# Kernel tuning notes

Hardware: AMD Instinct MI355X
Metric: run time of the kernel (lower is better)

The kernel has to match this reference:

```python
import jax, jax.numpy as jnp
import numpy as np

N_QUBITS = 8
N_LAYERS = 4
DIM = 2 ** N_QUBITS  # 256 state-vector

# PauliZ sign table: signs[i, idx] = +1 if bit of wire i in basis index idx is 0 else -1.
# Wire 0 is the most-significant axis (state axes ordered wire0..wire{n-1}).
_idx = np.arange(DIM)
SIGNS = np.stack([1.0 - 2.0 * ((_idx >> (N_QUBITS - 1 - i)) & 1) for i in range(N_QUBITS)]).astype(np.float32)  # [n, 256]


def _rx_mat(theta):
    c = jnp.cos(0.5 * theta).astype(jnp.complex64)
    s = (-1j * jnp.sin(0.5 * theta)).astype(jnp.complex64)
    return jnp.stack([jnp.stack([c, s]), jnp.stack([s, c])])  # [2,2]


def _rz_diag(theta):
    return jnp.stack([jnp.exp(-0.5j * theta), jnp.exp(0.5j * theta)]).astype(jnp.complex64)  # [2]


def _apply_1q(state, U, w):
    # state: (2,)*n complex64; apply 2x2 U on wire w
    st = jnp.moveaxis(state, w, 0).reshape(2, -1)
    st = U @ st
    return jnp.moveaxis(st.reshape((2,) * N_QUBITS), 0, w)


def _apply_diag(state, d, w):
    st = jnp.moveaxis(state, w, 0)
    st = st * d.reshape((2,) + (1,) * (N_QUBITS - 1))
    return jnp.moveaxis(st, 0, w)


def _cnot(state, c, t):
    st = jnp.moveaxis(state, (c, t), (0, 1))
    st = jnp.stack([st[0], st[1][::-1]], axis=0)  # flip target where control==1
    return jnp.moveaxis(st, (0, 1), (c, t))


def _circuit(angles, weights):
    # angles: [n_qubits], weights: [n_layers, 2, n_qubits] -> expvals [n_qubits]
    state = jnp.zeros((2,) * N_QUBITS, jnp.complex64).at[(0,) * N_QUBITS].set(1.0)
    for i in range(N_QUBITS):
        state = _apply_1q(state, _rx_mat(angles[i]), i)
        state = _apply_diag(state, _rz_diag(angles[i]), i)
    for l in range(N_LAYERS):
        for i in range(N_QUBITS):
            state = _apply_1q(state, _rx_mat(weights[l, 0, i]), i)
            state = _apply_diag(state, _rz_diag(weights[l, 1, i]), i)
        for i in range(N_QUBITS - 1):
            state = _cnot(state, i, i + 1)
    probs = jnp.abs(state.reshape(-1)) ** 2  # [256]
    return (probs @ SIGNS.T).astype(jnp.float32)  # [n_qubits] <Z_i>


def setup_inputs() -> dict:
    key = jax.random.key(0)
    B, D_IN, D_OUT = 8192, 1024, 1024
    ks = jax.random.split(key, 6)
    bound_in = np.sqrt(6.0 / D_IN)  # kaiming_uniform fan_in, linear
    bound_out = np.sqrt(6.0 / N_QUBITS)
    return {
        "x": jax.random.normal(ks[0], (B, D_IN), jnp.float32),
        "W_in": jax.random.uniform(ks[1], (N_QUBITS, D_IN), jnp.float32, -bound_in, bound_in),
        "b_in": jnp.zeros((N_QUBITS,), jnp.float32),
        "q_weights": jax.random.uniform(ks[2], (N_LAYERS, 2, N_QUBITS), jnp.float32, 0.0, 2.0 * np.pi),
        "W_out": jax.random.uniform(ks[3], (D_OUT, N_QUBITS), jnp.float32, -bound_out, bound_out),
        "b_out": jnp.zeros((D_OUT,), jnp.float32),
    }


def reference(x, W_in, b_in, q_weights, W_out, b_out):
    x_proj = x @ W_in.T + b_in                                   # [B, n_qubits]
    ev = jax.vmap(_circuit, in_axes=(0, None))(x_proj, q_weights)  # [B, n_qubits]
    return ev @ W_out.T + b_out                                   # [B, output_dim]
```

## Files before the change

### kernel.cpp

```cpp
#include <hip/hip_runtime.h>
#include <math.h>


typedef float f32x2 __attribute__((ext_vector_type(2)));

__device__ __forceinline__ int f2i(float v) { return __float_as_int(v); }
__device__ __forceinline__ float i2f(int v) { return __int_as_float(v); }

template <int CTRL>
__device__ __forceinline__ float dppf(float v) {
    return i2f(__builtin_amdgcn_update_dpp(0, f2i(v), CTRL, 0xF, 0xF, true));
}

template <int ML>
__device__ __forceinline__ float gshm(float v) {
    static_assert(ML > 0 && ML < 64, "lane mask");
    if constexpr (ML == 1)      return dppf<0xB1>(v);
    else if constexpr (ML == 2) return dppf<0x4E>(v);
    else if constexpr (ML == 3) return dppf<0x1B>(v);
    else if constexpr (ML == 8) return dppf<0x128>(v);
    else if constexpr (ML < 32) return i2f(__builtin_amdgcn_ds_swizzle(f2i(v), 0x1F | (ML << 10)));
    else                        return __shfl_xor(v, ML, 64);
}

template <int L>
__device__ __forceinline__ float rdlane(float v) {
    return i2f(__builtin_amdgcn_readlane(f2i(v), L));
}

template <int ML, int MR, int ZL, int ZR>
__device__ __forceinline__ void ggate(f32x2& reA, f32x2& reB, f32x2& imA, f32x2& imB,
                                      float c1, float s1, float c2, float s2,
                                      int lane) {
    f32x2 sReA, sReB, sImA, sImB;
    if constexpr (MR == 0)      { sReA = reA;    sReB = reB;    sImA = imA;    sImB = imB; }
    else if constexpr (MR == 1) { sReA = reA.yx; sReB = reB.yx; sImA = imA.yx; sImB = imB.yx; }
    else if constexpr (MR == 2) { sReA = reB;    sReB = reA;    sImA = imB;    sImB = imA; }
    else                        { sReA = reB.yx; sReB = reA.yx; sImA = imB.yx; sImB = imA.yx; }
    f32x2 pReA, pReB, pImA, pImB;
    if constexpr (ML != 0) {
        pReA.x = gshm<ML>(sReA.x); pReA.y = gshm<ML>(sReA.y);
        pReB.x = gshm<ML>(sReB.x); pReB.y = gshm<ML>(sReB.y);
        pImA.x = gshm<ML>(sImA.x); pImA.y = gshm<ML>(sImA.y);
        pImB.x = gshm<ML>(sImB.x); pImB.y = gshm<ML>(sImB.y);
    } else { pReA = sReA; pReB = sReB; pImA = sImA; pImB = sImB; }
    f32x2 nReA = c1 * reA + s1 * pImA;
    f32x2 nReB = c1 * reB + s1 * pImB;
    f32x2 nImA = c1 * imA - s1 * pReA;
    f32x2 nImB = c1 * imB - s1 * pReB;
    float base;
    if constexpr (ZL == 0) base = -s2;
    else                   base = (__popc(lane & ZL) & 1) ? s2 : -s2;
    constexpr bool N1 = (ZR & 1) != 0;
    constexpr bool N2 = ((ZR >> 1) & 1) != 0;
    constexpr bool N3 = (((ZR & 1) ^ ((ZR >> 1) & 1)) != 0);
    f32x2 ssA = { base, N1 ? -base : base };
    f32x2 ssB = { N2 ? -base : base, N3 ? -base : base };
    f32x2 tA = c2 * nReA - ssA * nImA;
    f32x2 tB = c2 * nReB - ssB * nImB;
    imA = c2 * nImA + ssA * nReA;
    imB = c2 * nImB + ssB * nReB;
    reA = tA;
    reB = tB;
}

__global__ void __launch_bounds__(256, 4) qasa_kernel(
    const float* __restrict__ x, const float* __restrict__ W_in,
    const float* __restrict__ b_in, const float* __restrict__ qw,
    const float* __restrict__ W_out, const float* __restrict__ b_out,
    float* __restrict__ out)
{
    const int tid = threadIdx.x;
    const int lane = tid & 63;
    const size_t row = (size_t)blockIdx.x * 4 + (tid >> 6);

    float vc, vs;
    __sincosf(0.5f * qw[lane], &vs, &vc);

    float acc[8] = {0.f, 0.f, 0.f, 0.f, 0.f, 0.f, 0.f, 0.f};
    {
        const float4* xr = (const float4*)(x + row * 1024);
        const float4* w4 = (const float4*)W_in;
#pragma unroll
        for (int k = 0; k < 4; ++k) {
            float4 xv = xr[lane + 64 * k];
#pragma unroll
            for (int q = 0; q < 8; ++q) {
                float4 wv = w4[q * 256 + lane + 64 * k];
                acc[q] += xv.x * wv.x + xv.y * wv.y + xv.z * wv.z + xv.w * wv.w;
            }
        }
    }
#pragma unroll
    for (int q = 0; q < 8; ++q) {
        acc[q] += dppf<0xB1>(acc[q]);
        acc[q] += dppf<0x4E>(acc[q]);
        acc[q] += dppf<0x128>(acc[q]);
    }
    const int b0 = lane & 1, b1 = (lane >> 1) & 1, b3 = (lane >> 3) & 1;
    float t01 = b0 ? acc[1] : acc[0];
    float t23 = b0 ? acc[3] : acc[2];
    float t45 = b0 ? acc[5] : acc[4];
    float t67 = b0 ? acc[7] : acc[6];
    float ta = b1 ? t23 : t01;
    float tb = b1 ? t67 : t45;
    float A = b3 ? tb : ta;
    A += gshm<4>(A); A += gshm<16>(A); A += gshm<32>(A);
    A += b_in[b0 | (b1 << 1) | (b3 << 2)];
    float ca, sa;
    __sincosf(0.5f * A, &sa, &ca);

    float ur = ca * ca, ui = -ca * sa, vr = sa * sa, vi = ui;
    const int q = b0 | (b1 << 1) | (b3 << 2);
    const int a1 = 4 * q, a2 = 4 * (q + 8);
    float cx = i2f(__builtin_amdgcn_ds_bpermute(a1, f2i(vc)));
    float sx = i2f(__builtin_amdgcn_ds_bpermute(a1, f2i(vs)));
    float cz = i2f(__builtin_amdgcn_ds_bpermute(a2, f2i(vc)));
    float sz = i2f(__builtin_amdgcn_ds_bpermute(a2, f2i(vs)));
    float ur1 = cx * ur + sx * vi, ui1 = cx * ui - sx * vr;
    float vr1 = cx * vr + sx * ui, vi1 = cx * vi - sx * ur;
    float ur2 = cz * ur1 + sz * ui1, ui2 = cz * ui1 - sz * ur1;
    float vr2 = cz * vr1 - sz * vi1, vi2 = cz * vi1 + sz * vr1;

    float Pr, Pi;
    {
        float fur = rdlane<0>(ur2), fui = rdlane<0>(ui2);
        float fvr = rdlane<0>(vr2), fvi = rdlane<0>(vi2);
        bool b = (lane >> 5) & 1;
        Pr = b ? fvr : fur;
        Pi = b ? fvi : fui;
    }
#define PMUL(W_, L_) { \
        float fur = rdlane<L_>(ur2), fui = rdlane<L_>(ui2); \
        float fvr = rdlane<L_>(vr2), fvi = rdlane<L_>(vi2); \
        bool b = (lane >> (5 - (W_))) & 1; \
        float fr = b ? fvr : fur, fi = b ? fvi : fui; \
        float tr = Pr * fr - Pi * fi; \
        Pi = Pr * fi + Pi * fr; \
        Pr = tr; }
    PMUL(1, 1) PMUL(2, 2) PMUL(3, 3) PMUL(4, 8) PMUL(5, 9)
#undef PMUL
    f32x2 reA, reB, imA, imB;
    {
        float u6r = rdlane<10>(ur2), u6i = rdlane<10>(ui2);
        float v6r = rdlane<10>(vr2), v6i = rdlane<10>(vi2);
        float u7r = rdlane<11>(ur2), u7i = rdlane<11>(ui2);
        float v7r = rdlane<11>(vr2), v7i = rdlane<11>(vi2);
        float rr[4], ii[4];
#pragma unroll
        for (int r = 0; r < 4; ++r) {
            float g6r_ = (r & 2) ? v6r : u6r, g6i_ = (r & 2) ? v6i : u6i;
            float g7r_ = (r & 1) ? v7r : u7r, g7i_ = (r & 1) ? v7i : u7i;
            float fr = g6r_ * g7r_ - g6i_ * g7i_;
            float fi = g6r_ * g7i_ + g6i_ * g7r_;
            rr[r] = Pr * fr - Pi * fi;
            ii[r] = Pr * fi + Pi * fr;
        }
        reA = (f32x2){ rr[0], rr[1] };  reB = (f32x2){ rr[2], rr[3] };
        imA = (f32x2){ ii[0], ii[1] };  imB = (f32x2){ ii[2], ii[3] };
    }

#define GG(Lx, W_, ML_, MR_, ZL_, ZR_) \
    ggate<ML_, MR_, ZL_, ZR_>(reA, reB, imA, imB, \
        rdlane<16 * (Lx) + (W_)>(vc), rdlane<16 * (Lx) + (W_)>(vs), \
        rdlane<16 * (Lx) + 8 + (W_)>(vc), rdlane<16 * (Lx) + 8 + (W_)>(vs), lane);

    GG(1,0, 48,0, 32,0)  GG(1,1, 24,0, 48,0)  GG(1,2, 12,0, 56,0) GG(1,3, 6,0, 60,0)
    GG(1,4, 3,0, 62,0)   GG(1,5, 1,2, 63,0)   GG(1,6, 0,3, 63,2)  GG(1,7, 0,1, 63,3)
    GG(2,0, 40,0, 32,0)  GG(2,1, 20,0, 16,0)  GG(2,2, 10,0, 40,0) GG(2,3, 5,0, 20,0)
    GG(2,4, 2,2, 42,0)   GG(2,5, 1,1, 21,0)   GG(2,6, 0,2, 42,2)  GG(2,7, 0,1, 21,1)
    GG(3,0, 60,0, 32,0)  GG(3,1, 30,0, 48,0)  GG(3,2, 15,0, 24,0) GG(3,3, 7,2, 12,0)
    GG(3,4, 3,3, 38,0)   GG(3,5, 1,3, 51,0)   GG(3,6, 0,3, 25,2)  GG(3,7, 0,1, 12,3)
#undef GG

    float p0 = reA.x * reA.x + imA.x * imA.x;
    float p1 = reA.y * reA.y + imA.y * imA.y;
    float p2 = reB.x * reB.x + imB.x * imB.x;
    float p3 = reB.y * reB.y + imB.y * imB.y;
    float q0 = (p0 + p1) + (p2 + p3);
    float q2 = (p0 + p1) - (p2 + p3);
    float q1 = (p0 + p2) - (p1 + p3);

    float v = q0;
    { float u = dppf<0xB1>(v);  v = (lane & 1)  ? (u - v) : (v + u); }
    { float u = dppf<0x4E>(v);  v = (lane & 2)  ? (u - v) : (v + u); }
    { float u = dppf<0x128>(v); v = (lane & 8)  ? (u - v) : (v + u); }
    { float u = gshm<4>(v);     v = (lane & 4)  ? (u - v) : (v + u); }
    { float u = gshm<16>(v);    v = (lane & 16) ? (u - v) : (v + u); }
    { float u = gshm<32>(v);    v = (lane & 32) ? (u - v) : (v + u); }
    const float EV0 = rdlane<32>(v), EV1 = rdlane<16>(v), EV2 = rdlane<8>(v);
    const float EV3 = rdlane<4>(v),  EV4 = rdlane<34>(v), EV5 = rdlane<17>(v);

    q2 += dppf<0xB1>(q2);
    q2 += dppf<0x4E>(q2);
    { float u = dppf<0x128>(q2); q2 = (lane & 8) ? (u - q2) : (q2 + u); }
    q2 += gshm<4>(q2); q2 += gshm<16>(q2); q2 += gshm<32>(q2);
    const float EV6 = rdlane<8>(q2);

    q1 += dppf<0xB1>(q1);
    q1 += dppf<0x4E>(q1);
    q1 += dppf<0x128>(q1);
    { float u = gshm<4>(q1); q1 = (lane & 4) ? (u - q1) : (q1 + u); }
    q1 += gshm<16>(q1); q1 += gshm<32>(q1);
    const float EV7 = rdlane<4>(q1);

    const f32x2 E01 = { EV0, EV1 }, E23 = { EV2, EV3 };
    const f32x2 E45 = { EV4, EV5 }, E67 = { EV6, EV7 };
    const float4* wo = (const float4*)W_out;
    const float4* bo = (const float4*)b_out;
    float4* orow = (float4*)(out + row * 1024);
#pragma unroll
    for (int jj = 0; jj < 4; ++jj) {
        const int c4 = lane + 64 * jj;
        float4 bias = bo[c4];
        float res[4];
#pragma unroll
        for (int c = 0; c < 4; ++c) {
            float4 wa = wo[2 * (4 * c4 + c)];
            float4 wb = wo[2 * (4 * c4 + c) + 1];
            f32x2 acc2 = E01 * (f32x2){ wa.x, wa.y } + E23 * (f32x2){ wa.z, wa.w }
                       + E45 * (f32x2){ wb.x, wb.y } + E67 * (f32x2){ wb.z, wb.w };
            res[c] = acc2.x + acc2.y;
        }
        float4 o;
        o.x = bias.x + res[0]; o.y = bias.y + res[1];
        o.z = bias.z + res[2]; o.w = bias.w + res[3];
        orow[c4] = o;
    }
}

extern "C" void kernel_launch(void* const* d_in, const int* in_sizes, int n_in,
                              void* d_out, int out_size, void* d_ws, size_t ws_size,
                              hipStream_t stream) {
    const float* x     = (const float*)d_in[0];
    const float* W_in  = (const float*)d_in[1];
    const float* b_in  = (const float*)d_in[2];
    const float* qw    = (const float*)d_in[3];
    const float* W_out = (const float*)d_in[4];
    const float* b_out = (const float*)d_in[5];
    float* outp = (float*)d_out;

    const int B = in_sizes[0] / 1024;
    const int grid = B / 4;
    qasa_kernel<<<grid, 256, 0, stream>>>(x, W_in, b_in, qw, W_out, b_out, outp);
}
```

Measured before the change: 124.9 us.

## Split input and output projections across warps with shared-memory exchange of angles

Each warp now computes two qubits' projections for all four rows of the block instead of all eight qubits for one row. This cuts per-warp W_in loads from eight vectors per k-step to two, while x loads rise from one to four. The partial angles are exchanged through shared memory behind a barrier. The output projection is likewise split by column slice: each warp loads a quarter of W_out once into registers and writes that slice for all four rows, reading expectation values from shared memory. The cost is two __syncthreads per block and some extra shared-memory traffic.

```diff
diff --git a/kernel.cpp b/kernel.cpp
--- a/kernel.cpp
+++ b/kernel.cpp
@@ -72,47 +72,61 @@
 {
     const int tid = threadIdx.x;
     const int lane = tid & 63;
-    const size_t row = (size_t)blockIdx.x * 4 + (tid >> 6);
+    const int w = tid >> 6;
+    const int block4 = blockIdx.x * 4;
+    const size_t row = (size_t)block4 + w;
+
+    __shared__ float ang[32];
+    __shared__ float evs[4][8] __attribute__((aligned(16)));
 
     float vc, vs;
     __sincosf(0.5f * qw[lane], &vs, &vc);
 
     float acc[8] = {0.f, 0.f, 0.f, 0.f, 0.f, 0.f, 0.f, 0.f};
     {
-        const float4* xr = (const float4*)(x + row * 1024);
         const float4* w4 = (const float4*)W_in;
+        const float4* xr0 = (const float4*)(x + (size_t)block4 * 1024);
 #pragma unroll
         for (int k = 0; k < 4; ++k) {
-            float4 xv = xr[lane + 64 * k];
-#pragma unroll
-            for (int q = 0; q < 8; ++q) {
-                float4 wv = w4[q * 256 + lane + 64 * k];
-                acc[q] += xv.x * wv.x + xv.y * wv.y + xv.z * wv.z + xv.w * wv.w;
+            float4 wv0 = w4[(2 * w) * 256 + lane + 64 * k];
+            float4 wv1 = w4[(2 * w + 1) * 256 + lane + 64 * k];
+#pragma unroll
+            for (int r = 0; r < 4; ++r) {
+                float4 xv = xr0[r * 256 + lane + 64 * k];
+                acc[r]     += xv.x * wv0.x + xv.y * wv0.y + xv.z * wv0.z + xv.w * wv0.w;
+                acc[4 + r] += xv.x * wv1.x + xv.y * wv1.y + xv.z * wv1.z + xv.w * wv1.w;
             }
         }
     }
 #pragma unroll
-    for (int q = 0; q < 8; ++q) {
-        acc[q] += dppf<0xB1>(acc[q]);
-        acc[q] += dppf<0x4E>(acc[q]);
-        acc[q] += dppf<0x128>(acc[q]);
+    for (int j = 0; j < 8; ++j) {
+        acc[j] += dppf<0xB1>(acc[j]);
+        acc[j] += dppf<0x4E>(acc[j]);
+        acc[j] += dppf<0x128>(acc[j]);
     }
     const int b0 = lane & 1, b1 = (lane >> 1) & 1, b3 = (lane >> 3) & 1;
-    float t01 = b0 ? acc[1] : acc[0];
-    float t23 = b0 ? acc[3] : acc[2];
-    float t45 = b0 ? acc[5] : acc[4];
-    float t67 = b0 ? acc[7] : acc[6];
-    float ta = b1 ? t23 : t01;
-    float tb = b1 ? t67 : t45;
-    float A = b3 ? tb : ta;
-    A += gshm<4>(A); A += gshm<16>(A); A += gshm<32>(A);
-    A += b_in[b0 | (b1 << 1) | (b3 << 2)];
+    {
+        float t01 = b0 ? acc[1] : acc[0];
+        float t23 = b0 ? acc[3] : acc[2];
+        float t45 = b0 ? acc[5] : acc[4];
+        float t67 = b0 ? acc[7] : acc[6];
+        float ta = b1 ? t23 : t01;
+        float tb = b1 ? t67 : t45;
+        float S = b3 ? tb : ta;
+        S += gshm<4>(S); S += gshm<16>(S); S += gshm<32>(S);
+        if ((lane & 52) == 0) {
+            int r = lane & 3, qp = (lane >> 3) & 1;
+            ang[(2 * w + qp) * 4 + r] = S;
+        }
+    }
+    __syncthreads();
+    const int qofl = b0 | (b1 << 1) | (b3 << 2);
+    float A = ang[qofl * 4 + w] + b_in[qofl];
     float ca, sa;
     __sincosf(0.5f * A, &sa, &ca);
 
     float ur = ca * ca, ui = -ca * sa, vr = sa * sa, vi = ui;
-    const int q = b0 | (b1 << 1) | (b3 << 2);
-    const int a1 = 4 * q, a2 = 4 * (q + 8);
+    const int a1 = 4 * qofl, a2 = 4 * (qofl + 8);
     float cx = i2f(__builtin_amdgcn_ds_bpermute(a1, f2i(vc)));
     float sx = i2f(__builtin_amdgcn_ds_bpermute(a1, f2i(vs)));
     float cz = i2f(__builtin_amdgcn_ds_bpermute(a2, f2i(vc)));
@@ -188,44 +202,58 @@
     { float u = gshm<4>(v);     v = (lane & 4)  ? (u - v) : (v + u); }
     { float u = gshm<16>(v);    v = (lane & 16) ? (u - v) : (v + u); }
     { float u = gshm<32>(v);    v = (lane & 32) ? (u - v) : (v + u); }
-    const float EV0 = rdlane<32>(v), EV1 = rdlane<16>(v), EV2 = rdlane<8>(v);
-    const float EV3 = rdlane<4>(v),  EV4 = rdlane<34>(v), EV5 = rdlane<17>(v);
 
     q2 += dppf<0xB1>(q2);
     q2 += dppf<0x4E>(q2);
     { float u = dppf<0x128>(q2); q2 = (lane & 8) ? (u - q2) : (q2 + u); }
     q2 += gshm<4>(q2); q2 += gshm<16>(q2); q2 += gshm<32>(q2);
-    const float EV6 = rdlane<8>(q2);
 
     q1 += dppf<0xB1>(q1);
     q1 += dppf<0x4E>(q1);
     q1 += dppf<0x128>(q1);
     { float u = gshm<4>(q1); q1 = (lane & 4) ? (u - q1) : (q1 + u); }
     q1 += gshm<16>(q1); q1 += gshm<32>(q1);
-    const float EV7 = rdlane<4>(q1);
-
-    const f32x2 E01 = { EV0, EV1 }, E23 = { EV2, EV3 };
-    const f32x2 E45 = { EV4, EV5 }, E67 = { EV6, EV7 };
-    const float4* wo = (const float4*)W_out;
-    const float4* bo = (const float4*)b_out;
-    float4* orow = (float4*)(out + row * 1024);
-#pragma unroll
-    for (int jj = 0; jj < 4; ++jj) {
-        const int c4 = lane + 64 * jj;
-        float4 bias = bo[c4];
-        float res[4];
+
+    {
+        const unsigned long long wrmask = 0x0000000500030110ULL;
+        if ((wrmask >> lane) & 1) {
+            int k = 6 - __ffs(lane);
+            evs[w][k] = v;
+        }
+        if (lane == 8 || lane == 4) {
+            evs[w][(lane == 8) ? 6 : 7] = (lane == 8) ? q2 : q1;
+        }
+    }
+    __syncthreads();
+
+    {
+        const int c4 = (w << 6) + lane;
+        const float4* wo = (const float4*)W_out;
+        float4 wa[4], wb[4];
 #pragma unroll
         for (int c = 0; c < 4; ++c) {
-            float4 wa = wo[2 * (4 * c4 + c)];
-            float4 wb = wo[2 * (4 * c4 + c) + 1];
-            f32x2 acc2 = E01 * (f32x2){ wa.x, wa.y } + E23 * (f32x2){ wa.z, wa.w }
-                       + E45 * (f32x2){ wb.x, wb.y } + E67 * (f32x2){ wb.z, wb.w };
-            res[c] = acc2.x + acc2.y;
-        }
-        float4 o;
-        o.x = bias.x + res[0]; o.y = bias.y + res[1];
-        o.z = bias.z + res[2]; o.w = bias.w + res[3];
-        orow[c4] = o;
+            wa[c] = wo[2 * (4 * c4 + c)];
+            wb[c] = wo[2 * (4 * c4 + c) + 1];
+        }
+        float4 bias = ((const float4*)b_out)[c4];
+#pragma unroll
+        for (int r = 0; r < 4; ++r) {
+            const float4* ev4 = (const float4*)evs[r];
+            float4 lo = ev4[0], hi = ev4[1];
+            f32x2 E01 = { lo.x, lo.y }, E23 = { lo.z, lo.w };
+            f32x2 E45 = { hi.x, hi.y }, E67 = { hi.z, hi.w };
+            float res[4];
+#pragma unroll
+            for (int c = 0; c < 4; ++c) {
+                f32x2 a2 = E01 * (f32x2){ wa[c].x, wa[c].y } + E23 * (f32x2){ wa[c].z, wa[c].w }
+                         + E45 * (f32x2){ wb[c].x, wb[c].y } + E67 * (f32x2){ wb[c].z, wb[c].w };
+                res[c] = a2.x + a2.y;
+            }
+            float4 o;
+            o.x = bias.x + res[0]; o.y = bias.y + res[1];
+            o.z = bias.z + res[2]; o.w = bias.w + res[3];
+            ((float4*)(out + (size_t)(block4 + r) * 1024))[c4] = o;
+        }
     }
 }
 
```

New measurement: 105.1 us. 15.8% less time.
